# Kernel tuning notes

Measured on AMD Instinct MI355X. Metric: run time of the kernel, lower is better.

Reference implementation:

```python
import jax, jax.numpy as jnp
import numpy as np

B, T, D, C = 2, 2048, 1024, 10
F = D // 2 + 1  # rfft bins; permutations act on frequency bins (perm_freq=True)


def setup_inputs() -> dict:
    key = jax.random.key(0)
    ks = jax.random.split(key, 6)
    s = 1.0 / np.sqrt(D)
    x = jax.random.normal(ks[0], (B, T, D), jnp.float32)
    Wq = jax.random.normal(ks[1], (D, D), jnp.float32) * s
    Wk = jax.random.normal(ks[2], (D, D), jnp.float32) * s
    Wv = jax.random.normal(ks[3], (D, D), jnp.float32) * s
    Wo = jax.random.normal(ks[4], (D, D), jnp.float32) * s
    # buffer: torch.randn(C, F).argsort(-1) -> random permutations of freq bins
    perms = jnp.argsort(jax.random.normal(ks[5], (C, F)), axis=-1)
    return {"x": x, "Wq": Wq, "Wk": Wk, "Wv": Wv, "Wo": Wo, "perms": perms}


def reference(x, Wq, Wk, Wv, Wo, perms):
    # linear projections (nn.Linear applies x @ W.T)
    q = x @ Wq.T
    k = x @ Wk.T
    v = x @ Wv.T
    # HRR bind/unbind in rfft frequency domain
    fq = jnp.fft.rfft(q, axis=-1)  # (B,T,F) complex
    fk = jnp.fft.rfft(k, axis=-1)
    fv = jnp.fft.rfft(v, axis=-1)
    # gather permuted redundant copies of freq bins: (B,T,C,F) -> (C,B,T,F)
    fkp = jnp.moveaxis(fk[..., perms], 2, 0)
    fqp = jnp.moveaxis(fq[..., perms], 2, 0)
    # causal associative memory: cumulative sum of key*value bindings over time
    kv = jnp.cumsum(fkp * fv[None], axis=-2)  # (C,B,T,F)
    # unbind with query (circular correlation = multiply by conj), mean copies
    r = jnp.mean(kv * jnp.conj(fqp), axis=0)  # (B,T,F)
    values_hat = jnp.fft.irfft(r, n=D, axis=-1)  # (B,T,D)
    return values_hat @ Wo.T
```

## Files before the change

### kernel.cpp

```cpp
#include <hip/hip_runtime.h>
#include <math.h>

#define B_   2
#define T_   2048
#define D_   1024
#define C_   10
#define F_   513
#define NTOK (B_ * T_)
#define LF   3078
#define LFP  3136
#define KP2  1056
#define NCH  128
#define TC   (T_ / NCH)

typedef unsigned short us16;
typedef __attribute__((ext_vector_type(8))) __bf16 bf16x8;
typedef __attribute__((ext_vector_type(4))) float  f32x4;

#define O_XBF    ((size_t)0)
#define O_PREP   ((size_t)8388608)
#define O_WT     (O_PREP)
#define O_WOBF   (O_PREP + 6291456)
#define O_TCS    (O_PREP + 8388608)
#define O_RCAT   (O_PREP)
#define O_SFB    (O_PREP + 10489856)
#define O_MALLB  (O_SFB + 2162688)
#define O_MOUTB  (O_MALLB + 6303744)
#define O_FALL   (O_MOUTB + 2162688)
#define O_SSCAN  (O_FALL + 25690112)

__device__ __forceinline__ us16 f2b(float f) {
    union { float f; unsigned u; } v; v.f = f;
    unsigned r = v.u + 0x7FFFu + ((v.u >> 16) & 1u);
    return (us16)(r >> 16);
}

__device__ __forceinline__ float2 b2f2(unsigned w) {
    union { unsigned u; float f; } a, b;
    a.u = (w & 0xffffu) << 16;
    b.u = w & 0xffff0000u;
    return make_float2(a.f, b.f);
}

__device__ __forceinline__ void gl_lds16(const us16* g, us16* l) {
    __builtin_amdgcn_global_load_lds(
        (const __attribute__((address_space(1))) unsigned*)g,
        (__attribute__((address_space(3))) unsigned*)l, 16, 0, 0);
}

__global__ void hrr_cvt_bf16(const float* __restrict__ in, us16* __restrict__ out, int n4) {
    int i = blockIdx.x * 256 + threadIdx.x;
    if (i < n4) {
        float4 v = ((const float4*)in)[i];
        ushort4 o;
        o.x = f2b(v.x); o.y = f2b(v.y); o.z = f2b(v.z); o.w = f2b(v.w);
        ((ushort4*)out)[i] = o;
    }
}

__global__ void hrr_transpose_bf16(const float* __restrict__ Wq,
                                   const float* __restrict__ Wk,
                                   const float* __restrict__ Wv,
                                   us16* __restrict__ WT) {
    const float* W = (blockIdx.z == 0) ? Wq : (blockIdx.z == 1) ? Wk : Wv;
    us16* O = WT + (size_t)blockIdx.z * D_ * D_;
    __shared__ float t[32][33];
    const int bx = blockIdx.x * 32, by = blockIdx.y * 32;
    const int tx = threadIdx.x & 31, ty = threadIdx.x >> 5;
#pragma unroll
    for (int i = 0; i < 32; i += 8)
        t[ty + i][tx] = W[(size_t)(by + ty + i) * D_ + bx + tx];
    __syncthreads();
#pragma unroll
    for (int i = 0; i < 32; i += 8)
        O[(size_t)(bx + ty + i) * D_ + by + tx] = f2b(t[tx][ty + i]);
}

__global__ void hrr_build_tcs(us16* __restrict__ Tcs) {
    int idx = blockIdx.x * 256 + threadIdx.x;
    if (idx >= 1026 * 1024) return;
    int r = idx >> 10, e = idx & 1023;
    int f = r >> 1;
    float ang = (float)((f * e) & 1023) * 6.135923151542565e-3f;
    Tcs[idx] = f2b((r & 1) ? -sinf(ang) : cosf(ang));
}

__global__ void hrr_build_sfb(us16* __restrict__ S) {
    int idx = blockIdx.x * 256 + threadIdx.x;
    if (idx >= KP2 * 1024) return;
    int r = idx >> 10, e = idx & 1023;
    float v = 0.f;
    if (r < 1026) {
        int f = r >> 1;
        float s = (f == 0 || f == 512) ? (1.0f / 1024.0f) : (2.0f / 1024.0f);
        float ang = (float)((f * e) & 1023) * 6.135923151542565e-3f;
        v = (r & 1) ? -s * sinf(ang) : s * cosf(ang);
    }
    S[idx] = f2b(v);
}

template <bool OUT_BF16>
__global__ __launch_bounds__(256, 3)
void hrr_gemm_mfma(const us16* __restrict__ Ab, const us16* __restrict__ Bb,
                   void* __restrict__ Cv, int M, int N, int K,
                   int lda, int ldb, int ldc, int Ncap,
                   size_t strideA, size_t strideB, size_t strideC) {
    const us16* A = Ab + strideA * blockIdx.z;
    const us16* B = Bb + strideB * blockIdx.z;

    __shared__ us16 smem[16384];
    us16* As = smem;
    us16* Bs = smem + 8192;

    const int tid  = threadIdx.x;
    const int lane = tid & 63;
    const int wave = tid >> 6;
    const int wm = (wave >> 1) * 64;
    const int wn = (wave & 1) * 64;
    const int bm = blockIdx.y * 128;
    const int bn = blockIdx.x * 128;

    const int r0    = tid >> 2;
    const int g_lds = tid & 3;
    const int g_src = g_lds ^ ((r0 >> 1) & 3);
    const int c4    = g_src * 8;

    int rA0 = bm + r0;      if (rA0 >= M) rA0 = M - 1;
    int rA1 = bm + 64 + r0; if (rA1 >= M) rA1 = M - 1;
    int rB0 = bn + r0;      if (rB0 >= N) rB0 = N - 1;
    int rB1 = bn + 64 + r0; if (rB1 >= N) rB1 = N - 1;
    const us16* pA0 = A + (size_t)rA0 * lda + c4;
    const us16* pA1 = A + (size_t)rA1 * lda + c4;
    const us16* pB0 = B + (size_t)rB0 * ldb + c4;
    const us16* pB1 = B + (size_t)rB1 * ldb + c4;

    f32x4 acc[4][4];
#pragma unroll
    for (int i = 0; i < 4; i++)
#pragma unroll
        for (int j = 0; j < 4; j++) acc[i][j] = (f32x4){0.f, 0.f, 0.f, 0.f};

    const int fr = lane & 15;
    const int gq = ((lane >> 4) ^ ((fr >> 1) & 3)) * 8;

    const int wb = wave * 512;
#define STAGE_TILE(buf, ko)                                  \
    do {                                                     \
        us16* a_ = As + (buf) * 4096 + wb;                   \
        us16* b_ = Bs + (buf) * 4096 + wb;                   \
        gl_lds16(pA0 + (ko), a_);                            \
        gl_lds16(pA1 + (ko), a_ + 2048);                     \
        gl_lds16(pB0 + (ko), b_);                            \
        gl_lds16(pB1 + (ko), b_ + 2048);                     \
    } while (0)

    STAGE_TILE(0, 0);
    __syncthreads();

    int cur = 0;
    for (int k0 = 0; k0 < K; k0 += 32) {
        const int kn = k0 + 32;
        if (kn < K) STAGE_TILE(cur ^ 1, kn);

        const us16* Ac = As + cur * 4096;
        const us16* Bc = Bs + cur * 4096;
        bf16x8 af[4], bfr[4];
#pragma unroll
        for (int i = 0; i < 4; i++)
            af[i] = *(const bf16x8*)(Ac + (wm + i * 16 + fr) * 32 + gq);
#pragma unroll
        for (int j = 0; j < 4; j++)
            bfr[j] = *(const bf16x8*)(Bc + (wn + j * 16 + fr) * 32 + gq);
#pragma unroll
        for (int i = 0; i < 4; i++)
#pragma unroll
            for (int j = 0; j < 4; j++)
                acc[i][j] = __builtin_amdgcn_mfma_f32_16x16x32_bf16(bfr[j], af[i], acc[i][j], 0, 0, 0);

        __syncthreads();
        cur ^= 1;
    }
#undef STAGE_TILE

    const int cl  = lane & 15;
    const int rq  = (lane >> 4) * 4;
    float* lbuf = (float*)smem;
#pragma unroll
    for (int p = 0; p < 4; ++p) {
        __syncthreads();
        if ((wave >> 1) == (p >> 1)) {
            const int ib = (p & 1) * 2;
#pragma unroll
            for (int ii = 0; ii < 2; ++ii) {
                const int rl = ii * 16 + cl;
#pragma unroll
                for (int j = 0; j < 4; ++j)
                    *(f32x4*)(lbuf + rl * 132 + wn + j * 16 + rq) = acc[ib + ii][j];
            }
        }
        __syncthreads();
        const int rbase = bm + p * 32;
        if (OUT_BF16) {
            us16* C = (us16*)Cv + strideC * blockIdx.z;
#pragma unroll
            for (int rr = 0; rr < 2; ++rr) {
                const int idx = rr * 2048 + tid * 8;
                const int row = idx >> 7, col = idx & 127;
                const int grow = rbase + row, gcol = bn + col;
                if (grow < M && gcol + 8 <= Ncap) {
                    const float* s = lbuf + row * 132 + col;
                    uint4 o;
                    o.x = (unsigned)f2b(s[0]) | ((unsigned)f2b(s[1]) << 16);
                    o.y = (unsigned)f2b(s[2]) | ((unsigned)f2b(s[3]) << 16);
                    o.z = (unsigned)f2b(s[4]) | ((unsigned)f2b(s[5]) << 16);
                    o.w = (unsigned)f2b(s[6]) | ((unsigned)f2b(s[7]) << 16);
                    *(uint4*)(C + (size_t)grow * ldc + gcol) = o;
                }
            }
        } else {
            float* C = (float*)Cv + strideC * blockIdx.z;
#pragma unroll
            for (int rr = 0; rr < 4; ++rr) {
                const int idx = rr * 1024 + tid * 4;
                const int row = idx >> 7, col = idx & 127;
                const int grow = rbase + row, gcol = bn + col;
                if (grow < M && gcol + 4 <= Ncap)
                    *(float4*)(C + (size_t)grow * ldc + gcol) =
                        *(const float4*)(lbuf + row * 132 + col);
            }
        }
    }
}

__global__ __launch_bounds__(256, 4)
void hrr_scan_sums(const us16* __restrict__ Fall, const int* __restrict__ perms,
                   float* __restrict__ S) {
    const int n = blockIdx.x, b = blockIdx.y, half = blockIdx.z;
    const int tid = threadIdx.x;
    const int f0 = half * 256;
    const int VL = half ? 257 : 256;
    __shared__ float2 kc[F_], vc[257];

    float aR[2][C_], aI[2][C_];
    int gg[2][C_];
#pragma unroll
    for (int i = 0; i < 2; i++) {
        const int f = (i == 0) ? (f0 + tid) : 512;
        const bool act = (i == 0) || (half == 1 && tid == 0);
#pragma unroll
        for (int c = 0; c < C_; c++) {
            gg[i][c] = act ? perms[c * F_ + f] : 0;
            aR[i][c] = aI[i][c] = 0.f;
        }
    }

    for (int tl = 0; tl < TC; tl++) {
        const us16* row = Fall + (size_t)(b * T_ + n * TC + tl) * LFP;
        __syncthreads();
        for (int j = tid; j < F_; j += 256)
            kc[j] = b2f2(*(const unsigned*)(row + 1026 + 2 * j));
        for (int j = tid; j < VL; j += 256)
            vc[j] = b2f2(*(const unsigned*)(row + 2052 + 2 * (f0 + j)));
        __syncthreads();
#pragma unroll
        for (int i = 0; i < 2; i++) {
            const int lv = (i == 0) ? tid : 256;
            if (i == 0 || (half == 1 && tid == 0)) {
                float2 v = vc[lv];
#pragma unroll
                for (int c = 0; c < C_; c++) {
                    float2 k = kc[gg[i][c]];
                    aR[i][c] += k.x * v.x - k.y * v.y;
                    aI[i][c] += k.x * v.y + k.y * v.x;
                }
            }
        }
    }
#pragma unroll
    for (int i = 0; i < 2; i++) {
        const int f = (i == 0) ? (f0 + tid) : 512;
        if (i == 0 || (half == 1 && tid == 0)) {
#pragma unroll
            for (int c = 0; c < C_; c++) {
                size_t a = ((((size_t)c * B_ + b) * NCH + n) * F_ + f) * 2;
                S[a] = aR[i][c]; S[a + 1] = aI[i][c];
            }
        }
    }
}

__global__ void hrr_scan_prefix(float* __restrict__ S) {
    int tid = blockIdx.x * 256 + threadIdx.x;
    if (tid >= C_ * B_ * F_) return;
    int c = tid / (B_ * F_);
    int r = tid % (B_ * F_);
    int b = r / F_, f = r % F_;
    size_t base = (((size_t)c * B_ + b) * NCH) * F_ + f;
    float runR = 0.f, runI = 0.f;
    for (int n0 = 0; n0 < NCH; n0 += 8) {
        float tR[8], tI[8];
#pragma unroll
        for (int u = 0; u < 8; u++) {
            size_t a = (base + (size_t)(n0 + u) * F_) * 2;
            tR[u] = S[a]; tI[u] = S[a + 1];
        }
#pragma unroll
        for (int u = 0; u < 8; u++) {
            size_t a = (base + (size_t)(n0 + u) * F_) * 2;
            S[a] = runR; S[a + 1] = runI;
            runR += tR[u]; runI += tI[u];
        }
    }
}

__global__ __launch_bounds__(256, 4)
void hrr_scan_apply(const us16* __restrict__ Fall, const int* __restrict__ perms,
                    const float* __restrict__ S, us16* __restrict__ Rcat) {
    const int n = blockIdx.x, b = blockIdx.y, half = blockIdx.z;
    const int tid = threadIdx.x;
    const int f0 = half * 256;
    const int VL = half ? 257 : 256;
    __shared__ float2 qc[F_], kc[F_], vc[257];

    float kvR[2][C_], kvI[2][C_];
    int gg[2][C_];
#pragma unroll
    for (int i = 0; i < 2; i++) {
        const int f = (i == 0) ? (f0 + tid) : 512;
        const bool act = (i == 0) || (half == 1 && tid == 0);
#pragma unroll
        for (int c = 0; c < C_; c++) {
            gg[i][c] = act ? perms[c * F_ + f] : 0;
            if (act) {
                size_t a = ((((size_t)c * B_ + b) * NCH + n) * F_ + f) * 2;
                kvR[i][c] = S[a]; kvI[i][c] = S[a + 1];
            } else { kvR[i][c] = 0.f; kvI[i][c] = 0.f; }
        }
    }

    for (int tl = 0; tl < TC; tl++) {
        const int tt = b * T_ + n * TC + tl;
        const us16* row = Fall + (size_t)tt * LFP;
        __syncthreads();
        for (int j = tid; j < F_; j += 256) {
            qc[j] = b2f2(*(const unsigned*)(row + 2 * j));
            kc[j] = b2f2(*(const unsigned*)(row + 1026 + 2 * j));
        }
        for (int j = tid; j < VL; j += 256)
            vc[j] = b2f2(*(const unsigned*)(row + 2052 + 2 * (f0 + j)));
        __syncthreads();
        unsigned* out32 = (unsigned*)(Rcat + (size_t)tt * KP2);
#pragma unroll
        for (int i = 0; i < 2; i++) {
            const int f = (i == 0) ? (f0 + tid) : 512;
            const int lv = (i == 0) ? tid : 256;
            if (i == 0 || (half == 1 && tid == 0)) {
                float2 v = vc[lv];
                float accR = 0.f, accI = 0.f;
#pragma unroll
                for (int c = 0; c < C_; c++) {
                    int g = gg[i][c];
                    float2 k = kc[g];
                    float nR = kvR[i][c] + k.x * v.x - k.y * v.y;
                    float nI = kvI[i][c] + k.x * v.y + k.y * v.x;
                    kvR[i][c] = nR; kvI[i][c] = nI;
                    float2 q = qc[g];
                    accR += nR * q.x + nI * q.y;
                    accI += nI * q.x - nR * q.y;
                }
                out32[f] = (unsigned)f2b(accR * 0.1f)
                         | ((unsigned)f2b(accI * 0.1f) << 16);
            }
        }
        if (half == 0 && tid < 15)
            out32[513 + tid] = 0;
    }
}

extern "C" void kernel_launch(void* const* d_in, const int* in_sizes, int n_in,
                              void* d_out, int out_size, void* d_ws, size_t ws_size,
                              hipStream_t stream) {
    const float* x  = (const float*)d_in[0];
    const float* Wq = (const float*)d_in[1];
    const float* Wk = (const float*)d_in[2];
    const float* Wv = (const float*)d_in[3];
    const float* Wo = (const float*)d_in[4];
    const int* perms = (const int*)d_in[5];
    float* out = (float*)d_out;

    char* ws = (char*)d_ws;
    us16* Xbf   = (us16*)(ws + O_XBF);
    us16* WT    = (us16*)(ws + O_WT);
    us16* WoBf  = (us16*)(ws + O_WOBF);
    us16* Tcs   = (us16*)(ws + O_TCS);
    us16* Sfb   = (us16*)(ws + O_SFB);
    us16* MallB = (us16*)(ws + O_MALLB);
    us16* MoutB = (us16*)(ws + O_MOUTB);
    us16* Rcat  = (us16*)(ws + O_RCAT);
    us16* Fall  = (us16*)(ws + O_FALL);
    float* Ssc  = (float*)(ws + O_SSCAN);

    hrr_cvt_bf16<<<4096, 256, 0, stream>>>(x, Xbf, NTOK * D_ / 4);
    hrr_cvt_bf16<<<1024, 256, 0, stream>>>(Wo, WoBf, D_ * D_ / 4);
    hrr_transpose_bf16<<<dim3(32, 32, 3), 256, 0, stream>>>(Wq, Wk, Wv, WT);
    hrr_build_tcs<<<(1026 * 1024 + 255) / 256, 256, 0, stream>>>(Tcs);
    hrr_build_sfb<<<(KP2 * 1024 + 255) / 256, 256, 0, stream>>>(Sfb);

    hrr_gemm_mfma<true><<<dim3(8, 9, 3), 256, 0, stream>>>(
        Tcs, WT, MallB, 1026, 1024, 1024, 1024, 1024, 1024, 1024,
        0, (size_t)D_ * D_, (size_t)1026 * 1024);

    hrr_gemm_mfma<true><<<dim3(9, 8, 1), 256, 0, stream>>>(
        WoBf, Sfb, MoutB, 1024, KP2, 1024, 1024, 1024, KP2, KP2, 0, 0, 0);

    hrr_gemm_mfma<true><<<dim3(25, 32, 1), 256, 0, stream>>>(
        Xbf, MallB, Fall, NTOK, LF, 1024, 1024, 1024, LFP, LFP, 0, 0, 0);

    hrr_scan_sums<<<dim3(NCH, B_, 2), 256, 0, stream>>>(Fall, perms, Ssc);
    hrr_scan_prefix<<<(C_ * B_ * F_ + 255) / 256, 256, 0, stream>>>(Ssc);
    hrr_scan_apply<<<dim3(NCH, B_, 2), 256, 0, stream>>>(Fall, perms, Ssc, Rcat);

    hrr_gemm_mfma<false><<<dim3(8, 32, 1), 256, 0, stream>>>(
        Rcat, MoutB, out, NTOK, D_, KP2, KP2, KP2, D_, D_, 0, 0, 0);
}
```

Baseline: 266.8 us.

## Fuse prep kernels and builder GEMMs, add XCD-aware block swizzle

Merges the five preprocessing kernels (bf16 conversions, weight transpose, DFT table builders) into one launch that dispatches on block-index ranges. The two constant-building GEMMs become one launch over a padded 9x9x4 grid, whose out-of-range tiles do wasted work and skip their writes. The two main GEMMs gain a block-index remap that groups neighbouring tiles onto the same XCD to improve L2 reuse. The aim is fewer launches and less serialisation of small kernels, at the cost of some idle tiles and branchy dispatch.

```diff
diff --git a/kernel.cpp b/kernel.cpp
--- a/kernel.cpp
+++ b/kernel.cpp
@@ -48,67 +48,66 @@
         (__attribute__((address_space(3))) unsigned*)l, 16, 0, 0);
 }
 
-__global__ void hrr_cvt_bf16(const float* __restrict__ in, us16* __restrict__ out, int n4) {
-    int i = blockIdx.x * 256 + threadIdx.x;
-    if (i < n4) {
-        float4 v = ((const float4*)in)[i];
+__global__ __launch_bounds__(256)
+void hrr_prep(const float* __restrict__ x,  const float* __restrict__ Wq,
+              const float* __restrict__ Wk, const float* __restrict__ Wv,
+              const float* __restrict__ Wo,
+              us16* __restrict__ Xbf, us16* __restrict__ WT,
+              us16* __restrict__ WoBf, us16* __restrict__ Tcs,
+              us16* __restrict__ Sfb) {
+    __shared__ float t[32][33];
+    const int bid = blockIdx.x, tid = threadIdx.x;
+    if (bid < 4096) {
+        int i = bid * 256 + tid;
+        float4 v = ((const float4*)x)[i];
         ushort4 o;
         o.x = f2b(v.x); o.y = f2b(v.y); o.z = f2b(v.z); o.w = f2b(v.w);
-        ((ushort4*)out)[i] = o;
-    }
-}
-
-__global__ void hrr_transpose_bf16(const float* __restrict__ Wq,
-                                   const float* __restrict__ Wk,
-                                   const float* __restrict__ Wv,
-                                   us16* __restrict__ WT) {
-    const float* W = (blockIdx.z == 0) ? Wq : (blockIdx.z == 1) ? Wk : Wv;
-    us16* O = WT + (size_t)blockIdx.z * D_ * D_;
-    __shared__ float t[32][33];
-    const int bx = blockIdx.x * 32, by = blockIdx.y * 32;
-    const int tx = threadIdx.x & 31, ty = threadIdx.x >> 5;
-#pragma unroll
-    for (int i = 0; i < 32; i += 8)
-        t[ty + i][tx] = W[(size_t)(by + ty + i) * D_ + bx + tx];
-    __syncthreads();
-#pragma unroll
-    for (int i = 0; i < 32; i += 8)
-        O[(size_t)(bx + ty + i) * D_ + by + tx] = f2b(t[tx][ty + i]);
-}
-
-__global__ void hrr_build_tcs(us16* __restrict__ Tcs) {
-    int idx = blockIdx.x * 256 + threadIdx.x;
-    if (idx >= 1026 * 1024) return;
-    int r = idx >> 10, e = idx & 1023;
-    int f = r >> 1;
-    float ang = (float)((f * e) & 1023) * 6.135923151542565e-3f;
-    Tcs[idx] = f2b((r & 1) ? -sinf(ang) : cosf(ang));
-}
-
-__global__ void hrr_build_sfb(us16* __restrict__ S) {
-    int idx = blockIdx.x * 256 + threadIdx.x;
-    if (idx >= KP2 * 1024) return;
-    int r = idx >> 10, e = idx & 1023;
-    float v = 0.f;
-    if (r < 1026) {
+        ((ushort4*)Xbf)[i] = o;
+    } else if (bid < 5120) {
+        int i = (bid - 4096) * 256 + tid;
+        float4 v = ((const float4*)Wo)[i];
+        ushort4 o;
+        o.x = f2b(v.x); o.y = f2b(v.y); o.z = f2b(v.z); o.w = f2b(v.w);
+        ((ushort4*)WoBf)[i] = o;
+    } else if (bid < 8192) {
+        const int l  = bid - 5120;
+        const int bz = l >> 10, l2 = l & 1023;
+        const int bx = (l2 & 31) * 32, by = (l2 >> 5) * 32;
+        const float* W = (bz == 0) ? Wq : (bz == 1) ? Wk : Wv;
+        us16* O = WT + (size_t)bz * D_ * D_;
+        const int tx = tid & 31, ty = tid >> 5;
+#pragma unroll
+        for (int i = 0; i < 32; i += 8)
+            t[ty + i][tx] = W[(size_t)(by + ty + i) * D_ + bx + tx];
+        __syncthreads();
+#pragma unroll
+        for (int i = 0; i < 32; i += 8)
+            O[(size_t)(bx + ty + i) * D_ + by + tx] = f2b(t[tx][ty + i]);
+    } else if (bid < 12296) {
+        int idx = (bid - 8192) * 256 + tid;
+        int r = idx >> 10, e = idx & 1023;
         int f = r >> 1;
-        float s = (f == 0 || f == 512) ? (1.0f / 1024.0f) : (2.0f / 1024.0f);
         float ang = (float)((f * e) & 1023) * 6.135923151542565e-3f;
-        v = (r & 1) ? -s * sinf(ang) : s * cosf(ang);
-    }
-    S[idx] = f2b(v);
+        Tcs[idx] = f2b((r & 1) ? -sinf(ang) : cosf(ang));
+    } else {
+        int idx = (bid - 12296) * 256 + tid;
+        int r = idx >> 10, e = idx & 1023;
+        float v = 0.f;
+        if (r < 1026) {
+            int f = r >> 1;
+            float s = (f == 0 || f == 512) ? (1.0f / 1024.0f) : (2.0f / 1024.0f);
+            float ang = (float)((f * e) & 1023) * 6.135923151542565e-3f;
+            v = (r & 1) ? -s * sinf(ang) : s * cosf(ang);
+        }
+        Sfb[idx] = f2b(v);
+    }
 }
 
 template <bool OUT_BF16>
-__global__ __launch_bounds__(256, 3)
-void hrr_gemm_mfma(const us16* __restrict__ Ab, const us16* __restrict__ Bb,
-                   void* __restrict__ Cv, int M, int N, int K,
-                   int lda, int ldb, int ldc, int Ncap,
-                   size_t strideA, size_t strideB, size_t strideC) {
-    const us16* A = Ab + strideA * blockIdx.z;
-    const us16* B = Bb + strideB * blockIdx.z;
-
-    __shared__ us16 smem[16384];
+__device__ __forceinline__ void gemm_core(
+    const us16* __restrict__ A, const us16* __restrict__ B, void* __restrict__ Cv,
+    int M, int N, int K, int lda, int ldb, int ldc, int Ncap,
+    int bm, int bn, us16* smem) {
     us16* As = smem;
     us16* Bs = smem + 8192;
 
@@ -117,8 +116,6 @@
     const int wave = tid >> 6;
     const int wm = (wave >> 1) * 64;
     const int wn = (wave & 1) * 64;
-    const int bm = blockIdx.y * 128;
-    const int bn = blockIdx.x * 128;
 
     const int r0    = tid >> 2;
     const int g_lds = tid & 3;
@@ -201,7 +198,7 @@
         __syncthreads();
         const int rbase = bm + p * 32;
         if (OUT_BF16) {
-            us16* C = (us16*)Cv + strideC * blockIdx.z;
+            us16* C = (us16*)Cv;
 #pragma unroll
             for (int rr = 0; rr < 2; ++rr) {
                 const int idx = rr * 2048 + tid * 8;
@@ -218,7 +215,7 @@
                 }
             }
         } else {
-            float* C = (float*)Cv + strideC * blockIdx.z;
+            float* C = (float*)Cv;
 #pragma unroll
             for (int rr = 0; rr < 4; ++rr) {
                 const int idx = rr * 1024 + tid * 4;
@@ -230,6 +227,40 @@
             }
         }
     }
+}
+
+template <bool OUT_BF16>
+__global__ __launch_bounds__(256, 3)
+void hrr_gemm(const us16* __restrict__ A, const us16* __restrict__ B,
+              void* __restrict__ C, int M, int N, int K,
+              int lda, int ldb, int ldc, int Ncap, int swz) {
+    __shared__ us16 smem[16384];
+    int bx = blockIdx.x, by = blockIdx.y;
+    if (swz) {
+        const int gx = gridDim.x;
+        const int id = bx + gx * by;
+        const int q = (gx * gridDim.y) >> 3;
+        const int nid = (id & 7) * q + (id >> 3);
+        bx = nid % gx; by = nid / gx;
+    }
+    gemm_core<OUT_BF16>(A, B, C, M, N, K, lda, ldb, ldc, Ncap,
+                        by * 128, bx * 128, smem);
+}
+
+__global__ __launch_bounds__(256, 3)
+void hrr_gemm_builders(const us16* __restrict__ Tcs, const us16* __restrict__ WT,
+                       us16* __restrict__ MallB, const us16* __restrict__ WoBf,
+                       const us16* __restrict__ Sfb, us16* __restrict__ MoutB) {
+    __shared__ us16 smem[16384];
+    const int bm = blockIdx.y * 128, bn = blockIdx.x * 128;
+    const int z = blockIdx.z;
+    if (z < 3)
+        gemm_core<true>(Tcs, WT + (size_t)z * D_ * D_,
+                        MallB + (size_t)z * 1026 * 1024,
+                        1026, 1024, 1024, 1024, 1024, 1024, 1024, bm, bn, smem);
+    else
+        gemm_core<true>(WoBf, Sfb, MoutB,
+                        1024, KP2, 1024, 1024, 1024, KP2, KP2, bm, bn, smem);
 }
 
 __global__ __launch_bounds__(256, 4)
@@ -400,26 +431,17 @@
     us16* Fall  = (us16*)(ws + O_FALL);
     float* Ssc  = (float*)(ws + O_SSCAN);
 
-    hrr_cvt_bf16<<<4096, 256, 0, stream>>>(x, Xbf, NTOK * D_ / 4);
-    hrr_cvt_bf16<<<1024, 256, 0, stream>>>(Wo, WoBf, D_ * D_ / 4);
-    hrr_transpose_bf16<<<dim3(32, 32, 3), 256, 0, stream>>>(Wq, Wk, Wv, WT);
-    hrr_build_tcs<<<(1026 * 1024 + 255) / 256, 256, 0, stream>>>(Tcs);
-    hrr_build_sfb<<<(KP2 * 1024 + 255) / 256, 256, 0, stream>>>(Sfb);
-
-    hrr_gemm_mfma<true><<<dim3(8, 9, 3), 256, 0, stream>>>(
-        Tcs, WT, MallB, 1026, 1024, 1024, 1024, 1024, 1024, 1024,
-        0, (size_t)D_ * D_, (size_t)1026 * 1024);
-
-    hrr_gemm_mfma<true><<<dim3(9, 8, 1), 256, 0, stream>>>(
-        WoBf, Sfb, MoutB, 1024, KP2, 1024, 1024, 1024, KP2, KP2, 0, 0, 0);
-
-    hrr_gemm_mfma<true><<<dim3(25, 32, 1), 256, 0, stream>>>(
-        Xbf, MallB, Fall, NTOK, LF, 1024, 1024, 1024, LFP, LFP, 0, 0, 0);
+    hrr_prep<<<16520, 256, 0, stream>>>(x, Wq, Wk, Wv, Wo, Xbf, WT, WoBf, Tcs, Sfb);
+
+    hrr_gemm_builders<<<dim3(9, 9, 4), 256, 0, stream>>>(Tcs, WT, MallB, WoBf, Sfb, MoutB);
+
+    hrr_gemm<true><<<dim3(25, 32), 256, 0, stream>>>(
+        Xbf, MallB, Fall, NTOK, LF, 1024, 1024, 1024, LFP, LFP, 1);
 
     hrr_scan_sums<<<dim3(NCH, B_, 2), 256, 0, stream>>>(Fall, perms, Ssc);
     hrr_scan_prefix<<<(C_ * B_ * F_ + 255) / 256, 256, 0, stream>>>(Ssc);
     hrr_scan_apply<<<dim3(NCH, B_, 2), 256, 0, stream>>>(Fall, perms, Ssc, Rcat);
 
-    hrr_gemm_mfma<false><<<dim3(8, 32, 1), 256, 0, stream>>>(
-        Rcat, MoutB, out, NTOK, D_, KP2, KP2, KP2, D_, D_, 0, 0, 0);
-}
+    hrr_gemm<false><<<dim3(8, 32), 256, 0, stream>>>(
+        Rcat, MoutB, out, NTOK, D_, KP2, KP2, KP2, D_, D_, 1);
+}
```

Measured after the change: 243.3 us. 8.8% less time.
